# Kernel optimization log

Hardware: AMD Instinct MI355X
Metric: run time of the kernel (lower is better)

Reference implementation:

```python
import jax, jax.numpy as jnp
import numpy as np

B, T = 32, 2048
HID, ACT, SRC, AGE = 512, 64, 2, 16
TRUNK, BINS, PHASES = 256, 20, 7
IN_DIM = HID + ACT + SRC + AGE  # 594


def setup_inputs() -> dict:
    key = jax.random.key(0)
    ks = jax.random.split(key, 16)
    s_in = 1.0 / np.sqrt(IN_DIM)
    s_tr = 1.0 / np.sqrt(TRUNK)
    s_h = 1.0 / np.sqrt(HID)
    return {
        "h_t": jax.random.normal(ks[0], (B, T, HID), jnp.float32),
        "a_t": jax.random.normal(ks[1], (B, T, ACT), jnp.float32),
        "d_t": jax.random.normal(ks[2], (B, T, SRC), jnp.float32),
        "age_embed": jax.random.normal(ks[3], (B, T, AGE), jnp.float32),
        "trunk_w": jax.random.normal(ks[4], (IN_DIM, TRUNK), jnp.float32) * s_in,
        "trunk_b": jax.random.normal(ks[5], (TRUNK,), jnp.float32) * s_in,
        "inst_base_w": jax.random.normal(ks[6], (TRUNK, BINS), jnp.float32) * s_tr,
        "inst_base_b": jax.random.normal(ks[7], (BINS,), jnp.float32) * s_tr,
        "group_base_w": jax.random.normal(ks[8], (TRUNK, BINS), jnp.float32) * s_tr,
        "group_base_b": jax.random.normal(ks[9], (BINS,), jnp.float32) * s_tr,
        "inst_exp_w": jax.random.normal(ks[10], (PHASES, TRUNK, BINS), jnp.float32) * s_tr,
        "inst_exp_b": jax.random.normal(ks[11], (PHASES, BINS), jnp.float32) * s_tr,
        "group_exp_w": jax.random.normal(ks[12], (PHASES, TRUNK, BINS), jnp.float32) * s_tr,
        "group_exp_b": jax.random.normal(ks[13], (PHASES, BINS), jnp.float32) * s_tr,
        "router_w": jax.random.normal(ks[14], (HID, PHASES), jnp.float32) * s_h,
        "router_b": jax.random.normal(ks[15], (PHASES,), jnp.float32) * s_h,
    }


def reference(h_t, a_t, d_t, age_embed,
              trunk_w, trunk_b, inst_base_w, inst_base_b,
              group_base_w, group_base_b, inst_exp_w, inst_exp_b,
              group_exp_w, group_exp_b, router_w, router_b):
    # Shared trunk: Linear(594,256) -> exact GELU
    x = jnp.concatenate([h_t, a_t, d_t, age_embed], axis=-1)  # [B,T,594]
    z = jax.nn.gelu(jnp.einsum('bti,io->bto', x, trunk_w) + trunk_b,
                    approximate=False)  # [B,T,256]

    # Soft phase routing from h_t
    pw = jax.nn.softmax(jnp.einsum('bth,hp->btp', h_t, router_w) + router_b,
                        axis=-1)  # [B,T,7]

    # Base heads
    inst_base = jnp.einsum('btd,dk->btk', z, inst_base_w) + inst_base_b
    group_base = jnp.einsum('btd,dk->btk', z, group_base_w) + group_base_b

    # All 7 experts as one batched GEMM, then weighted reduction over phases
    inst_e = jnp.einsum('btd,pdk->btpk', z, inst_exp_w) + inst_exp_b  # [B,T,7,20]
    group_e = jnp.einsum('btd,pdk->btpk', z, group_exp_w) + group_exp_b
    inst_res = jnp.einsum('btp,btpk->btk', pw, inst_e)
    group_res = jnp.einsum('btp,btpk->btk', pw, group_e)

    return (inst_base + inst_res, group_base + group_res)
```

## Files before the change

### kernel.cpp

```cpp
#include <hip/hip_runtime.h>
#include <math.h>

typedef unsigned int uint;
typedef unsigned short ushort;

using short8 = __attribute__((ext_vector_type(8))) short;
using f32x4  = __attribute__((ext_vector_type(4))) float;

#define BT      65536
#define HID     512
#define IN_DIM  594
#define TRUNK   256
#define BINS    20
#define NCOMBO  320

#define WT_P_SZ (19*16*64*8)
#define RP_SZ   (16*64*8)
#define WA_P_SZ (8*20*64*8)

__device__ inline ushort f2bf(float f) {
    uint u = __float_as_uint(f);
    return (ushort)((u + 0x7fffu + ((u >> 16) & 1u)) >> 16);
}

__global__ __launch_bounds__(64) void pack_all(
    const float* __restrict__ trunk_w, const float* __restrict__ router_w,
    const float* __restrict__ inst_base_w, const float* __restrict__ inst_base_b,
    const float* __restrict__ group_base_w, const float* __restrict__ group_base_b,
    const float* __restrict__ inst_exp_w, const float* __restrict__ inst_exp_b,
    const float* __restrict__ group_exp_w, const float* __restrict__ group_exp_b,
    ushort* __restrict__ WtP, ushort* __restrict__ RP,
    ushort* __restrict__ WaP, float* __restrict__ wbias)
{
    const int b = blockIdx.x, l = threadIdx.x;
    const int lr = l & 15, lg = l >> 4;
    if (b < 304) {
        int kk = b >> 4, n = b & 15;
        int col = n * 16 + lr;
        ushort* dst = WtP + ((size_t)(kk * 16 + n) * 64 + l) * 8;
        #pragma unroll
        for (int j = 0; j < 8; ++j) {
            int k = kk * 32 + lg * 8 + j;
            dst[j] = (k < IN_DIM) ? f2bf(trunk_w[k * TRUNK + col]) : (ushort)0;
        }
    } else if (b < 320) {
        int kk = b - 304;
        ushort* dst = RP + ((size_t)(kk * 64 + l)) * 8;
        #pragma unroll
        for (int j = 0; j < 8; ++j) {
            int k = kk * 32 + lg * 8 + j;
            dst[j] = (lr < 7) ? f2bf(router_w[k * 7 + lr]) : (ushort)0;
        }
    } else if (b < 480) {
        int b2 = b - 320, kk = b2 / 20, n = b2 % 20;
        int combo = n * 16 + lr;
        int h = combo / 160, rem = combo % 160, kb = rem >> 3, p = rem & 7;
        const float* bw = h ? group_base_w : inst_base_w;
        const float* ew = h ? group_exp_w  : inst_exp_w;
        ushort* dst = WaP + ((size_t)(kk * 20 + n) * 64 + l) * 8;
        #pragma unroll
        for (int j = 0; j < 8; ++j) {
            int k = kk * 32 + lg * 8 + j;
            float v = (p == 0) ? bw[k * BINS + kb]
                               : ew[((p - 1) * TRUNK + k) * BINS + kb];
            dst[j] = f2bf(v);
        }
    } else {
        for (int c = l; c < NCOMBO; c += 64) {
            int h = c / 160, rem = c % 160, kb = rem >> 3, p = rem & 7;
            const float* bb = h ? group_base_b : inst_base_b;
            const float* eb = h ? group_exp_b  : inst_exp_b;
            wbias[c] = (p == 0) ? bb[kb] : eb[(p - 1) * BINS + kb];
        }
    }
}

__global__ __launch_bounds__(256, 2) void fused_mfma(
    const float* __restrict__ h_t, const float* __restrict__ a_t,
    const float* __restrict__ d_t, const float* __restrict__ age,
    const float* __restrict__ trunk_b, const float* __restrict__ router_b,
    const ushort* __restrict__ WtP, const ushort* __restrict__ RP,
    const ushort* __restrict__ WaP, const float* __restrict__ wbias,
    float* __restrict__ out)
{
    __shared__ alignas(16) ushort zs[32768];

    const int tid = threadIdx.x;
    const int l = tid & 63, w = tid >> 6;
    const int lr = l & 15, lg = l >> 4;
    const int block0 = blockIdx.x * 128;

    const int srow = tid >> 1;
    const int half = tid & 1;
    const size_t stok = block0 + srow;

    ushort* xs = zs;

    f32x4 acc[8][4];
    f32x4 accr0 = (f32x4){0.f,0.f,0.f,0.f};
    f32x4 accr1 = (f32x4){0.f,0.f,0.f,0.f};
    #pragma unroll
    for (int mm = 0; mm < 8; ++mm)
    #pragma unroll
    for (int nn = 0; nn < 4; ++nn) acc[mm][nn] = (f32x4){0.f,0.f,0.f,0.f};

    auto stage_load = [&](int kk, float4 ld[4]) {
        if (kk < 16) {
            const float4* p = (const float4*)(h_t + stok * HID + kk * 32 + half * 16);
            ld[0]=p[0]; ld[1]=p[1]; ld[2]=p[2]; ld[3]=p[3];
        } else if (kk < 18) {
            const float4* p = (const float4*)(a_t + stok * 64 + (kk - 16) * 32 + half * 16);
            ld[0]=p[0]; ld[1]=p[1]; ld[2]=p[2]; ld[3]=p[3];
        } else {
            float* f = (float*)ld;
            #pragma unroll
            for (int j = 0; j < 16; ++j) {
                int c = 576 + half * 16 + j;
                float v;
                if (c < 578)      v = d_t[stok * 2 + (c - 576)];
                else if (c < 594) v = age[stok * 16 + (c - 578)];
                else              v = 0.f;
                f[j] = v;
            }
        }
    };
    auto stage_write = [&](int buf, float4 ld[4]) {
        const float* f = (const float*)ld;
        short8 v0, v1;
        #pragma unroll
        for (int j = 0; j < 8; ++j) {
            v0[j] = (short)f2bf(f[j]);
            v1[j] = (short)f2bf(f[j + 8]);
        }
        ushort* dst = xs + buf * 4096 + (srow >> 4) * 512 + ((srow & 15) + half * 32) * 8;
        *(short8*)dst = v0;
        *(short8*)(dst + 128) = v1;
    };

    {
        float4 ld[4];
        stage_load(0, ld);
        stage_write(0, ld);
        __syncthreads();
        int cur = 0;
        const int w4 = w * 4;
        #pragma unroll 1
        for (int kk = 0; kk < 19; ++kk) {
            float4 nld[4];
            if (kk < 18) stage_load(kk + 1, nld);

            const ushort* wp = WtP + ((size_t)kk * 16 + w4) * 512;
            short8 bq0 = *(const short8*)(wp + 0 * 512 + l * 8);
            short8 bq1 = *(const short8*)(wp + 1 * 512 + l * 8);
            short8 bq2 = *(const short8*)(wp + 2 * 512 + l * 8);
            short8 bq3 = *(const short8*)(wp + 3 * 512 + l * 8);

            const ushort* xb = xs + cur * 4096;
            short8 a0 = *(const short8*)(xb + 0 * 512 + l * 8);
            short8 a1 = *(const short8*)(xb + 1 * 512 + l * 8);
            short8 a2 = *(const short8*)(xb + 2 * 512 + l * 8);
            short8 a3 = *(const short8*)(xb + 3 * 512 + l * 8);
            short8 a4 = *(const short8*)(xb + 4 * 512 + l * 8);
            short8 a5 = *(const short8*)(xb + 5 * 512 + l * 8);
            short8 a6 = *(const short8*)(xb + 6 * 512 + l * 8);
            short8 a7 = *(const short8*)(xb + 7 * 512 + l * 8);

            if (kk < 16) {
                short8 rb = *(const short8*)(RP + (size_t)kk * 512 + l * 8);
                short8 ar0 = *(const short8*)(xb + (w * 2 + 0) * 512 + l * 8);
                short8 ar1 = *(const short8*)(xb + (w * 2 + 1) * 512 + l * 8);
                accr0 = __builtin_amdgcn_mfma_f32_16x16x32_bf16(ar0, rb, accr0, 0, 0, 0);
                accr1 = __builtin_amdgcn_mfma_f32_16x16x32_bf16(ar1, rb, accr1, 0, 0, 0);
            }

            #define TRUNK_MM(AF) \
                acc[0][0] = __builtin_amdgcn_mfma_f32_16x16x32_bf16(AF, bq0, acc[0][0],0,0,0);
            #undef TRUNK_MM
            #pragma unroll
            for (int nn = 0; nn < 4; ++nn) {
                short8 bq = (nn == 0) ? bq0 : (nn == 1) ? bq1 : (nn == 2) ? bq2 : bq3;
                acc[0][nn] = __builtin_amdgcn_mfma_f32_16x16x32_bf16(a0, bq, acc[0][nn],0,0,0);
                acc[1][nn] = __builtin_amdgcn_mfma_f32_16x16x32_bf16(a1, bq, acc[1][nn],0,0,0);
                acc[2][nn] = __builtin_amdgcn_mfma_f32_16x16x32_bf16(a2, bq, acc[2][nn],0,0,0);
                acc[3][nn] = __builtin_amdgcn_mfma_f32_16x16x32_bf16(a3, bq, acc[3][nn],0,0,0);
                acc[4][nn] = __builtin_amdgcn_mfma_f32_16x16x32_bf16(a4, bq, acc[4][nn],0,0,0);
                acc[5][nn] = __builtin_amdgcn_mfma_f32_16x16x32_bf16(a5, bq, acc[5][nn],0,0,0);
                acc[6][nn] = __builtin_amdgcn_mfma_f32_16x16x32_bf16(a6, bq, acc[6][nn],0,0,0);
                acc[7][nn] = __builtin_amdgcn_mfma_f32_16x16x32_bf16(a7, bq, acc[7][nn],0,0,0);
            }

            if (kk < 18) stage_write(cur ^ 1, nld);
            __syncthreads();
            cur ^= 1;
        }
    }

    float pwv[2][4];
    {
        const float rb_l = (lr < 7) ? router_b[lr] : 0.f;
        #pragma unroll
        for (int m = 0; m < 2; ++m)
        #pragma unroll
        for (int r = 0; r < 4; ++r) {
            float lv = (m == 0) ? accr0[r] : accr1[r];
            float x = (lr < 7) ? (lv + rb_l) : -3.0e38f;
            float mx = x;
            mx = fmaxf(mx, __shfl_xor(mx, 1));
            mx = fmaxf(mx, __shfl_xor(mx, 2));
            mx = fmaxf(mx, __shfl_xor(mx, 4));
            mx = fmaxf(mx, __shfl_xor(mx, 8));
            float e = expf(x - mx);
            float s = e;
            s += __shfl_xor(s, 1);
            s += __shfl_xor(s, 2);
            s += __shfl_xor(s, 4);
            s += __shfl_xor(s, 8);
            pwv[m][r] = e / s;
        }
    }

    {
        char* zb = (char*)zs;
        #pragma unroll
        for (int nn = 0; nn < 4; ++nn) {
            float tb = trunk_b[(w * 4 + nn) * 16 + lr];
            int colbase = (w * 4 + nn) * 16 + lr;
            #pragma unroll
            for (int mm = 0; mm < 8; ++mm)
            #pragma unroll
            for (int r = 0; r < 4; ++r) {
                float v = acc[mm][nn][r] + tb;
                v = 0.5f * v * (1.f + erff(v * 0.70710678118654752f));
                int row  = mm * 16 + lg * 4 + r;
                int slot = (colbase >> 3) ^ (row & 7);
                *(ushort*)(zb + row * 512 + slot * 16 + (colbase & 7) * 2) = f2bf(v);
            }
        }
    }
    __syncthreads();

    const char* zb = (const char*)zs;
    const int p8 = l & 7;
    const int csrc = (l & 48) | (p8 ? (p8 - 1) : 0);
    const int row0 = w * 32 + lr;
    const int row1 = row0 + 16;

    float cw[2][4];
    #pragma unroll
    for (int m = 0; m < 2; ++m)
    #pragma unroll
    for (int r = 0; r < 4; ++r)
        cw[m][r] = __shfl(pwv[m][r], csrc);

    #pragma unroll 1
    for (int hf = 0; hf < 2; ++hf) {
        f32x4 acc2[2][10];
        #pragma unroll
        for (int m = 0; m < 2; ++m)
        #pragma unroll
        for (int n = 0; n < 10; ++n) acc2[m][n] = (f32x4){0.f,0.f,0.f,0.f};
        float wb_[10];
        #pragma unroll
        for (int n = 0; n < 10; ++n) wb_[n] = wbias[(hf * 10 + n) * 16 + lr];

        #pragma unroll
        for (int kk = 0; kk < 8; ++kk) {
            short8 a0 = *(const short8*)(zb + row0 * 512 + (((kk * 4 + lg) ^ (row0 & 7)) << 4));
            short8 a1 = *(const short8*)(zb + row1 * 512 + (((kk * 4 + lg) ^ (row1 & 7)) << 4));
            const ushort* wp = WaP + (size_t)(kk * 20 + hf * 10) * 512;
            #pragma unroll
            for (int n = 0; n < 10; ++n) {
                short8 bq = *(const short8*)(wp + (size_t)n * 512 + l * 8);
                acc2[0][n] = __builtin_amdgcn_mfma_f32_16x16x32_bf16(a0, bq, acc2[0][n],0,0,0);
                acc2[1][n] = __builtin_amdgcn_mfma_f32_16x16x32_bf16(a1, bq, acc2[1][n],0,0,0);
            }
        }

        #pragma unroll
        for (int m = 0; m < 2; ++m)
        #pragma unroll
        for (int n = 0; n < 10; ++n)
        #pragma unroll
        for (int r = 0; r < 4; ++r) {
            float e = acc2[m][n][r] + wb_[n];
            float val = (p8 ? cw[m][r] : 1.0f) * e;
            val += __shfl_xor(val, 1);
            val += __shfl_xor(val, 2);
            val += __shfl_xor(val, 4);
            if (p8 == 0) {
                int combo = (hf * 10 + n) * 16 + lr;
                int h = combo / 160, rem = combo % 160, kb = rem >> 3;
                size_t t = block0 + w * 32 + m * 16 + lg * 4 + r;
                out[(size_t)h * (BT * BINS) + t * BINS + kb] = val;
            }
        }
    }
}

extern "C" void kernel_launch(void* const* d_in, const int* in_sizes, int n_in,
                              void* d_out, int out_size, void* d_ws, size_t ws_size,
                              hipStream_t stream) {
    const float* h_t          = (const float*)d_in[0];
    const float* a_t          = (const float*)d_in[1];
    const float* d_t          = (const float*)d_in[2];
    const float* age_embed    = (const float*)d_in[3];
    const float* trunk_w      = (const float*)d_in[4];
    const float* trunk_b      = (const float*)d_in[5];
    const float* inst_base_w  = (const float*)d_in[6];
    const float* inst_base_b  = (const float*)d_in[7];
    const float* group_base_w = (const float*)d_in[8];
    const float* group_base_b = (const float*)d_in[9];
    const float* inst_exp_w   = (const float*)d_in[10];
    const float* inst_exp_b   = (const float*)d_in[11];
    const float* group_exp_w  = (const float*)d_in[12];
    const float* group_exp_b  = (const float*)d_in[13];
    const float* router_w     = (const float*)d_in[14];
    const float* router_b     = (const float*)d_in[15];

    ushort* WtP   = (ushort*)d_ws;
    ushort* RP    = WtP + WT_P_SZ;
    ushort* WaP   = RP + RP_SZ;
    float*  wbias = (float*)(WaP + WA_P_SZ);

    pack_all<<<481, 64, 0, stream>>>(
        trunk_w, router_w,
        inst_base_w, inst_base_b, group_base_w, group_base_b,
        inst_exp_w, inst_exp_b, group_exp_w, group_exp_b,
        WtP, RP, WaP, wbias);

    fused_mfma<<<BT / 128, 256, 0, stream>>>(
        h_t, a_t, d_t, age_embed, trunk_b, router_b,
        WtP, RP, WaP, wbias, (float*)d_out);
}
```

Measured before the change: 92.76 us.

## Split fused kernel into trunk and head kernels with global z staging

Splits the single fused kernel into a trunk kernel and a head kernel. The trunk kernel loads inputs straight from global memory into MFMA fragments with no LDS double-buffer, and each wave handles 16 tokens across all 256 columns. It writes GELU'd z in bf16 fragment layout plus the softmax routing weights to workspace, and the head kernel then runs the expert GEMMs and the phase reduction. It also switches to packed bf16 conversion intrinsics. This aims for higher occupancy and simpler pipelines, at the cost of an extra 32 MB z round trip through global memory and one more kernel launch. A fallback keeps the fused path when the workspace is too small.

Result: slower. 158.8 us (+71.2%).

```diff
diff --git a/kernel.cpp b/kernel.cpp
--- a/kernel.cpp
+++ b/kernel.cpp
@@ -1,4 +1,5 @@
 #include <hip/hip_runtime.h>
+#include <hip/hip_bf16.h>
 #include <math.h>
 
 typedef unsigned int uint;
@@ -17,10 +18,27 @@
 #define WT_P_SZ (19*16*64*8)
 #define RP_SZ   (16*64*8)
 #define WA_P_SZ (8*20*64*8)
+#define OFF_WBIAS  491520u
+#define OFF_PWG    492800u
+#define OFF_ZFRAG  2589952u
+#define WS_NEED    (OFF_ZFRAG + (size_t)BT * TRUNK * 2)
 
 __device__ inline ushort f2bf(float f) {
     uint u = __float_as_uint(f);
     return (ushort)((u + 0x7fffu + ((u >> 16) & 1u)) >> 16);
+}
+__device__ inline uint pk2(float lo, float hi) {
+    union { __hip_bfloat162 b; uint u; } cv;
+    cv.b = __float22bfloat162_rn(float2{lo, hi});
+    return cv.u;
+}
+__device__ inline short8 cvt8pk(float4 a, float4 b) {
+    union { uint4 t; short8 s; } cv;
+    cv.t.x = pk2(a.x, a.y);
+    cv.t.y = pk2(a.z, a.w);
+    cv.t.z = pk2(b.x, b.y);
+    cv.t.w = pk2(b.z, b.w);
+    return cv.s;
 }
 
 __global__ __launch_bounds__(64) void pack_all(
@@ -75,7 +93,187 @@
     }
 }
 
-__global__ __launch_bounds__(256, 2) void fused_mfma(
+__global__ __launch_bounds__(256, 3) void trunk_kernel(
+    const float* __restrict__ h_t, const float* __restrict__ a_t,
+    const float* __restrict__ d_t, const float* __restrict__ age,
+    const float* __restrict__ trunk_b, const float* __restrict__ router_b,
+    const ushort* __restrict__ WtP, const ushort* __restrict__ RP,
+    ushort* __restrict__ zfrag, float* __restrict__ pwg)
+{
+    __shared__ alignas(16) ushort zsh[64 * 256];
+
+    const int tid = threadIdx.x;
+    const int l = tid & 63, w = tid >> 6;
+    const int lr = l & 15, lg = l >> 4;
+    const int block0 = blockIdx.x * 64;
+    const size_t tok = block0 + w * 16 + lr;
+
+    f32x4 acc[16];
+    f32x4 accr = (f32x4){0.f,0.f,0.f,0.f};
+    #pragma unroll
+    for (int nf = 0; nf < 16; ++nf) acc[nf] = (f32x4){0.f,0.f,0.f,0.f};
+
+    #pragma unroll 2
+    for (int kk = 0; kk < 16; ++kk) {
+        const float4* p = (const float4*)(h_t + tok * HID + kk * 32 + lg * 8);
+        float4 f0 = p[0], f1 = p[1];
+        short8 a = cvt8pk(f0, f1);
+        short8 rb = *(const short8*)(RP + (size_t)kk * 512 + l * 8);
+        accr = __builtin_amdgcn_mfma_f32_16x16x32_bf16(a, rb, accr, 0, 0, 0);
+        const ushort* wp = WtP + (size_t)kk * 16 * 512;
+        #pragma unroll
+        for (int nf = 0; nf < 16; ++nf) {
+            short8 bq = *(const short8*)(wp + (size_t)nf * 512 + l * 8);
+            acc[nf] = __builtin_amdgcn_mfma_f32_16x16x32_bf16(a, bq, acc[nf], 0, 0, 0);
+        }
+    }
+    #pragma unroll
+    for (int kk = 16; kk < 18; ++kk) {
+        const float4* p = (const float4*)(a_t + tok * 64 + (kk - 16) * 32 + lg * 8);
+        float4 f0 = p[0], f1 = p[1];
+        short8 a = cvt8pk(f0, f1);
+        const ushort* wp = WtP + (size_t)kk * 16 * 512;
+        #pragma unroll
+        for (int nf = 0; nf < 16; ++nf) {
+            short8 bq = *(const short8*)(wp + (size_t)nf * 512 + l * 8);
+            acc[nf] = __builtin_amdgcn_mfma_f32_16x16x32_bf16(a, bq, acc[nf], 0, 0, 0);
+        }
+    }
+    {
+        float f[8];
+        #pragma unroll
+        for (int j = 0; j < 8; ++j) {
+            int c = 576 + lg * 8 + j;
+            float v;
+            if (c < 578)      v = d_t[tok * 2 + (c - 576)];
+            else if (c < 594) v = age[tok * 16 + (c - 578)];
+            else              v = 0.f;
+            f[j] = v;
+        }
+        short8 a = cvt8pk(float4{f[0],f[1],f[2],f[3]}, float4{f[4],f[5],f[6],f[7]});
+        const ushort* wp = WtP + (size_t)18 * 16 * 512;
+        #pragma unroll
+        for (int nf = 0; nf < 16; ++nf) {
+            short8 bq = *(const short8*)(wp + (size_t)nf * 512 + l * 8);
+            acc[nf] = __builtin_amdgcn_mfma_f32_16x16x32_bf16(a, bq, acc[nf], 0, 0, 0);
+        }
+    }
+
+    {
+        const float rb_l = (lr < 7) ? router_b[lr] : 0.f;
+        #pragma unroll
+        for (int r = 0; r < 4; ++r) {
+            float x = (lr < 7) ? (accr[r] + rb_l) : -3.0e38f;
+            float mx = x;
+            mx = fmaxf(mx, __shfl_xor(mx, 1));
+            mx = fmaxf(mx, __shfl_xor(mx, 2));
+            mx = fmaxf(mx, __shfl_xor(mx, 4));
+            mx = fmaxf(mx, __shfl_xor(mx, 8));
+            float e = expf(x - mx);
+            float s = e;
+            s += __shfl_xor(s, 1);
+            s += __shfl_xor(s, 2);
+            s += __shfl_xor(s, 4);
+            s += __shfl_xor(s, 8);
+            if (lr < 7)
+                pwg[(size_t)(block0 + w * 16 + lg * 4 + r) * 8 + lr] = e / s;
+        }
+    }
+
+    {
+        char* zb = (char*)zsh;
+        #pragma unroll
+        for (int nf = 0; nf < 16; ++nf) {
+            int col = nf * 16 + lr;
+            float tb = trunk_b[col];
+            #pragma unroll
+            for (int r = 0; r < 4; ++r) {
+                float v = acc[nf][r] + tb;
+                v = 0.5f * v * (1.f + erff(v * 0.70710678118654752f));
+                int row  = w * 16 + lg * 4 + r;
+                int slot = (col >> 3) ^ (row & 7);
+                *(ushort*)(zb + row * 512 + slot * 16 + (col & 7) * 2) = f2bf(v);
+            }
+        }
+    }
+
+    {
+        const char* zb = (const char*)zsh;
+        const int row = w * 16 + lr;
+        #pragma unroll
+        for (int kk2 = 0; kk2 < 8; ++kk2) {
+            short8 zv = *(const short8*)(zb + row * 512 + (((kk2 * 4 + lg) ^ (row & 7)) << 4));
+            *(short8*)(zfrag + (((size_t)(blockIdx.x * 4 + w) * 8 + kk2) * 64 + l) * 8) = zv;
+        }
+    }
+}
+
+__global__ __launch_bounds__(256, 3) void head_kernel(
+    const ushort* __restrict__ WaP, const float* __restrict__ wbias,
+    const ushort* __restrict__ zfrag, const float* __restrict__ pwg,
+    float* __restrict__ out)
+{
+    const int tid = threadIdx.x;
+    const int l = tid & 63, w = tid >> 6;
+    const int lr = l & 15, lg = l >> 4;
+    const int block0 = blockIdx.x * 64;
+    const int p8 = l & 7;
+    const int psel = p8 ? (p8 - 1) : 0;
+
+    f32x4 acc2[4][5];
+    #pragma unroll
+    for (int mm = 0; mm < 4; ++mm)
+    #pragma unroll
+    for (int nn = 0; nn < 5; ++nn) acc2[mm][nn] = (f32x4){0.f,0.f,0.f,0.f};
+
+    #pragma unroll
+    for (int kk2 = 0; kk2 < 8; ++kk2) {
+        short8 a[4];
+        #pragma unroll
+        for (int mm = 0; mm < 4; ++mm)
+            a[mm] = *(const short8*)(zfrag
+                + (((size_t)(blockIdx.x * 4 + mm) * 8 + kk2) * 64 + l) * 8);
+        const ushort* wp = WaP + ((size_t)kk2 * 20 + w * 5) * 512;
+        #pragma unroll
+        for (int nn = 0; nn < 5; ++nn) {
+            short8 bq = *(const short8*)(wp + (size_t)nn * 512 + l * 8);
+            acc2[0][nn] = __builtin_amdgcn_mfma_f32_16x16x32_bf16(a[0], bq, acc2[0][nn],0,0,0);
+            acc2[1][nn] = __builtin_amdgcn_mfma_f32_16x16x32_bf16(a[1], bq, acc2[1][nn],0,0,0);
+            acc2[2][nn] = __builtin_amdgcn_mfma_f32_16x16x32_bf16(a[2], bq, acc2[2][nn],0,0,0);
+            acc2[3][nn] = __builtin_amdgcn_mfma_f32_16x16x32_bf16(a[3], bq, acc2[3][nn],0,0,0);
+        }
+    }
+
+    float cwv[4][4];
+    #pragma unroll
+    for (int mm = 0; mm < 4; ++mm)
+    #pragma unroll
+    for (int r = 0; r < 4; ++r)
+        cwv[mm][r] = pwg[(size_t)(block0 + mm * 16 + lg * 4 + r) * 8 + psel];
+
+    #pragma unroll
+    for (int nn = 0; nn < 5; ++nn) {
+        int combo = (w * 5 + nn) * 16 + lr;
+        float wb = wbias[combo];
+        int h = combo / 160, rem = combo % 160, kb = rem >> 3;
+        #pragma unroll
+        for (int mm = 0; mm < 4; ++mm)
+        #pragma unroll
+        for (int r = 0; r < 4; ++r) {
+            float e = acc2[mm][nn][r] + wb;
+            float val = (p8 ? cwv[mm][r] : 1.0f) * e;
+            val += __shfl_xor(val, 1);
+            val += __shfl_xor(val, 2);
+            val += __shfl_xor(val, 4);
+            if (p8 == 0) {
+                size_t t = block0 + mm * 16 + lg * 4 + r;
+                out[(size_t)h * (BT * BINS) + t * BINS + kb] = val;
+            }
+        }
+    }
+}
+
+__global__ __launch_bounds__(256, 2) void fused_fallback(
     const float* __restrict__ h_t, const float* __restrict__ a_t,
     const float* __restrict__ d_t, const float* __restrict__ age,
     const float* __restrict__ trunk_b, const float* __restrict__ router_b,
@@ -89,11 +287,9 @@
     const int l = tid & 63, w = tid >> 6;
     const int lr = l & 15, lg = l >> 4;
     const int block0 = blockIdx.x * 128;
-
     const int srow = tid >> 1;
     const int half = tid & 1;
     const size_t stok = block0 + srow;
-
     ushort* xs = zs;
 
     f32x4 acc[8][4];
@@ -125,13 +321,8 @@
         }
     };
     auto stage_write = [&](int buf, float4 ld[4]) {
-        const float* f = (const float*)ld;
-        short8 v0, v1;
-        #pragma unroll
-        for (int j = 0; j < 8; ++j) {
-            v0[j] = (short)f2bf(f[j]);
-            v1[j] = (short)f2bf(f[j + 8]);
-        }
+        short8 v0 = cvt8pk(ld[0], ld[1]);
+        short8 v1 = cvt8pk(ld[2], ld[3]);
         ushort* dst = xs + buf * 4096 + (srow >> 4) * 512 + ((srow & 15) + half * 32) * 8;
         *(short8*)dst = v0;
         *(short8*)(dst + 128) = v1;
@@ -148,13 +339,11 @@
         for (int kk = 0; kk < 19; ++kk) {
             float4 nld[4];
             if (kk < 18) stage_load(kk + 1, nld);
-
             const ushort* wp = WtP + ((size_t)kk * 16 + w4) * 512;
             short8 bq0 = *(const short8*)(wp + 0 * 512 + l * 8);
             short8 bq1 = *(const short8*)(wp + 1 * 512 + l * 8);
             short8 bq2 = *(const short8*)(wp + 2 * 512 + l * 8);
             short8 bq3 = *(const short8*)(wp + 3 * 512 + l * 8);
-
             const ushort* xb = xs + cur * 4096;
             short8 a0 = *(const short8*)(xb + 0 * 512 + l * 8);
             short8 a1 = *(const short8*)(xb + 1 * 512 + l * 8);
@@ -164,7 +353,6 @@
             short8 a5 = *(const short8*)(xb + 5 * 512 + l * 8);
             short8 a6 = *(const short8*)(xb + 6 * 512 + l * 8);
             short8 a7 = *(const short8*)(xb + 7 * 512 + l * 8);
-
             if (kk < 16) {
                 short8 rb = *(const short8*)(RP + (size_t)kk * 512 + l * 8);
                 short8 ar0 = *(const short8*)(xb + (w * 2 + 0) * 512 + l * 8);
@@ -172,10 +360,6 @@
                 accr0 = __builtin_amdgcn_mfma_f32_16x16x32_bf16(ar0, rb, accr0, 0, 0, 0);
                 accr1 = __builtin_amdgcn_mfma_f32_16x16x32_bf16(ar1, rb, accr1, 0, 0, 0);
             }
-
-            #define TRUNK_MM(AF) \
-                acc[0][0] = __builtin_amdgcn_mfma_f32_16x16x32_bf16(AF, bq0, acc[0][0],0,0,0);
-            #undef TRUNK_MM
             #pragma unroll
             for (int nn = 0; nn < 4; ++nn) {
                 short8 bq = (nn == 0) ? bq0 : (nn == 1) ? bq1 : (nn == 2) ? bq2 : bq3;
@@ -188,7 +372,6 @@
                 acc[6][nn] = __builtin_amdgcn_mfma_f32_16x16x32_bf16(a6, bq, acc[6][nn],0,0,0);
                 acc[7][nn] = __builtin_amdgcn_mfma_f32_16x16x32_bf16(a7, bq, acc[7][nn],0,0,0);
             }
-
             if (kk < 18) stage_write(cur ^ 1, nld);
             __syncthreads();
             cur ^= 1;
@@ -223,8 +406,8 @@
         char* zb = (char*)zs;
         #pragma unroll
         for (int nn = 0; nn < 4; ++nn) {
-            float tb = trunk_b[(w * 4 + nn) * 16 + lr];
             int colbase = (w * 4 + nn) * 16 + lr;
+            float tb = trunk_b[colbase];
             #pragma unroll
             for (int mm = 0; mm < 8; ++mm)
             #pragma unroll
@@ -317,10 +500,11 @@
     const float* router_w     = (const float*)d_in[14];
     const float* router_b     = (const float*)d_in[15];
 
-    ushort* WtP   = (ushort*)d_ws;
+    char* ws = (char*)d_ws;
+    ushort* WtP   = (ushort*)ws;
     ushort* RP    = WtP + WT_P_SZ;
     ushort* WaP   = RP + RP_SZ;
-    float*  wbias = (float*)(WaP + WA_P_SZ);
+    float*  wbias = (float*)(ws + OFF_WBIAS);
 
     pack_all<<<481, 64, 0, stream>>>(
         trunk_w, router_w,
@@ -328,7 +512,17 @@
         inst_exp_w, inst_exp_b, group_exp_w, group_exp_b,
         WtP, RP, WaP, wbias);
 
-    fused_mfma<<<BT / 128, 256, 0, stream>>>(
-        h_t, a_t, d_t, age_embed, trunk_b, router_b,
-        WtP, RP, WaP, wbias, (float*)d_out);
-}
+    if (ws_size >= WS_NEED) {
+        float*  pwg   = (float*)(ws + OFF_PWG);
+        ushort* zfrag = (ushort*)(ws + OFF_ZFRAG);
+        trunk_kernel<<<BT / 64, 256, 0, stream>>>(
+            h_t, a_t, d_t, age_embed, trunk_b, router_b,
+            WtP, RP, zfrag, pwg);
+        head_kernel<<<BT / 64, 256, 0, stream>>>(
+            WaP, wbias, zfrag, pwg, (float*)d_out);
+    } else {
+        fused_fallback<<<BT / 128, 256, 0, stream>>>(
+            h_t, a_t, d_t, age_embed, trunk_b, router_b,
+            WtP, RP, WaP, wbias, (float*)d_out);
+    }
+}
```
